# Optimization experiments

Measured on AMD Instinct MI355X. Metric: run time of the kernel, lower is better.

Reference implementation:

```python
import jax, jax.numpy as jnp
import numpy as np

A0 = 0.5291772105638411
KE = 14.399645351950548
KEHALF = KE / 2.0


def _softplus_inverse(x):
    return float(np.log(np.expm1(x)))


def setup_inputs() -> dict:
    key = jax.random.key(0)
    k_nb, k_mask, k_z, k_r = jax.random.split(key, 4)
    B, A, K = 16, 1024, 1023
    neighbors = jax.random.randint(k_nb, (B, A, K), 0, A)
    neighbor_mask = (jax.random.uniform(k_mask, (B, A, K)) > 0.1).astype(jnp.float32)
    atomic_numbers = jax.random.randint(k_z, (B, A), 1, 95)
    r_ij = jax.random.uniform(k_r, (B, A, K), minval=0.5, maxval=10.0, dtype=jnp.float32)
    p = jnp.float32
    params = {
        "_adiv": jnp.full((1,), _softplus_inverse(1.0 / (0.8854 * A0)), p),
        "_apow": jnp.full((1,), _softplus_inverse(0.23), p),
        "_c1": jnp.full((1,), _softplus_inverse(0.1818), p),
        "_c2": jnp.full((1,), _softplus_inverse(0.5099), p),
        "_c3": jnp.full((1,), _softplus_inverse(0.2802), p),
        "_c4": jnp.full((1,), _softplus_inverse(0.02817), p),
        "_a1": jnp.full((1,), _softplus_inverse(3.2), p),
        "_a2": jnp.full((1,), _softplus_inverse(0.9423), p),
        "_a3": jnp.full((1,), _softplus_inverse(0.4028), p),
        "_a4": jnp.full((1,), _softplus_inverse(0.2016), p),
    }
    return dict(neighbors=neighbors, neighbor_mask=neighbor_mask,
                atomic_numbers=atomic_numbers, r_ij=r_ij, **params)


def reference(neighbors, neighbor_mask, atomic_numbers, r_ij,
              _adiv, _apow, _c1, _c2, _c3, _c4, _a1, _a2, _a3, _a4):
    sp = jax.nn.softplus
    B = neighbors.shape[0]
    Zf = atomic_numbers.astype(jnp.float32)            # [B, A]
    Zp = Zf ** sp(_apow)                               # [B, A] (param [1] broadcasts)
    bidx = jnp.arange(B)[:, None, None]                # batch index for gather
    # gather of symmetric pair quantities without materializing [B, A, A]:
    # a[b,i,j] = Zp[b,i] + Zp[b,j];  zizj[b,i,j] = Zf[b,i] * Zf[b,j]
    Zp_j = Zp[bidx, neighbors]                         # [B, A, K]
    Zf_j = Zf[bidx, neighbors]                         # [B, A, K]
    a = (Zp[:, :, None] + Zp_j) * sp(_adiv) * neighbor_mask
    zizj = Zf[:, :, None] * Zf_j * neighbor_mask
    # normalized mixture coefficients
    c1, c2, c3, c4 = sp(_c1), sp(_c2), sp(_c3), sp(_c4)
    csum = c1 + c2 + c3 + c4
    c1, c2, c3, c4 = c1 / csum, c2 / csum, c3 / csum, c4 / csum
    ar = a * r_ij
    f = (c1 * jnp.exp(-sp(_a1) * ar) + c2 * jnp.exp(-sp(_a2) * ar)
         + c3 * jnp.exp(-sp(_a3) * ar) + c4 * jnp.exp(-sp(_a4) * ar))
    valid = neighbor_mask != 0
    r_safe = jnp.where(valid, r_ij, 1.0)
    corr_ij = jnp.where(valid, KEHALF * f * zizj / r_safe, 0.0)
    return jnp.sum(corr_ij, axis=-1, keepdims=True)    # [B, A, 1]
```

## Files before the change

### kernel.cpp

```cpp
#include <hip/hip_runtime.h>
#include <math.h>

#define KEHALF_F 7.199822675975274f

__device__ __forceinline__ float softplus_f(float x) {
    return log1pf(__expf(x));
}

__global__ __launch_bounds__(256) void zbl_precompute_kernel(
    const int* __restrict__ atomic_numbers,
    const float* __restrict__ p_adiv, const float* __restrict__ p_apow,
    const float* __restrict__ p_c1, const float* __restrict__ p_c2,
    const float* __restrict__ p_c3, const float* __restrict__ p_c4,
    const float* __restrict__ p_a1, const float* __restrict__ p_a2,
    const float* __restrict__ p_a3, const float* __restrict__ p_a4,
    float* __restrict__ ws, int n)
{
    int idx = blockIdx.x * blockDim.x + threadIdx.x;
    float sp_apow = softplus_f(p_apow[0]);
    if (idx == 0) {
        float c1 = softplus_f(p_c1[0]), c2 = softplus_f(p_c2[0]);
        float c3 = softplus_f(p_c3[0]), c4 = softplus_f(p_c4[0]);
        float cs = c1 + c2 + c3 + c4;
        ws[0] = softplus_f(p_adiv[0]);
        ws[1] = c1 / cs; ws[2] = c2 / cs; ws[3] = c3 / cs; ws[4] = c4 / cs;
        ws[5] = softplus_f(p_a1[0]); ws[6] = softplus_f(p_a2[0]);
        ws[7] = softplus_f(p_a3[0]); ws[8] = softplus_f(p_a4[0]);
    }
    if (idx < n) {
        float zf = (float)atomic_numbers[idx];
        ws[16 + idx] = powf(zf, sp_apow);
    }
}

__global__ __launch_bounds__(256) void zbl_main_kernel(
    const int* __restrict__ neighbors,
    const float* __restrict__ neighbor_mask,
    const int* __restrict__ atomic_numbers,
    const float* __restrict__ r_ij,
    const float* __restrict__ ws,
    float* __restrict__ out,
    int A, int K)
{
    __shared__ float2 zz[1024];
    __shared__ float wsum[4];

    const int row = blockIdx.x;
    const int b   = row / A;
    const int i   = row - b * A;

    const float* zp_row = ws + 16 + (size_t)b * A;
    const int*   z_row  = atomic_numbers + (size_t)b * A;
    for (int t = threadIdx.x; t < A; t += 256) {
        zz[t] = make_float2((float)z_row[t], zp_row[t]);
    }
    __syncthreads();

    const float sp_adiv = ws[0];
    const float c1 = ws[1], c2 = ws[2], c3 = ws[3], c4 = ws[4];
    const float a1 = ws[5], a2 = ws[6], a3 = ws[7], a4 = ws[8];

    const float2 zi = zz[i];

    const size_t base = (size_t)row * K;
    const int*   nb = neighbors     + base;
    const float* mk = neighbor_mask + base;
    const float* rr = r_ij          + base;

    float acc = 0.0f;
    for (int k = threadIdx.x; k < K; k += 256) {
        int   j = nb[k];
        float m = mk[k];
        float r = rr[k];
        float2 zj = zz[j];
        float am = (zi.y + zj.y) * sp_adiv * m;
        float ar = am * r;
        float f = c1 * __expf(-a1 * ar) + c2 * __expf(-a2 * ar)
                + c3 * __expf(-a3 * ar) + c4 * __expf(-a4 * ar);
        float zizj = zi.x * zj.x * m;
        acc += f * __fdividef(zizj, r);
    }
    acc *= KEHALF_F;

    #pragma unroll
    for (int off = 32; off > 0; off >>= 1)
        acc += __shfl_down(acc, off, 64);
    const int lane = threadIdx.x & 63;
    const int wid  = threadIdx.x >> 6;
    if (lane == 0) wsum[wid] = acc;
    __syncthreads();
    if (threadIdx.x == 0)
        out[row] = wsum[0] + wsum[1] + wsum[2] + wsum[3];
}

extern "C" void kernel_launch(void* const* d_in, const int* in_sizes, int n_in,
                              void* d_out, int out_size, void* d_ws, size_t ws_size,
                              hipStream_t stream) {
    const int*   neighbors      = (const int*)  d_in[0];
    const float* neighbor_mask  = (const float*)d_in[1];
    const int*   atomic_numbers = (const int*)  d_in[2];
    const float* r_ij           = (const float*)d_in[3];
    const float* p_adiv = (const float*)d_in[4];
    const float* p_apow = (const float*)d_in[5];
    const float* p_c1   = (const float*)d_in[6];
    const float* p_c2   = (const float*)d_in[7];
    const float* p_c3   = (const float*)d_in[8];
    const float* p_c4   = (const float*)d_in[9];
    const float* p_a1   = (const float*)d_in[10];
    const float* p_a2   = (const float*)d_in[11];
    const float* p_a3   = (const float*)d_in[12];
    const float* p_a4   = (const float*)d_in[13];

    float* out = (float*)d_out;
    float* ws  = (float*)d_ws;

    const int n = in_sizes[2];
    const int A = 1024;
    const int K = in_sizes[0] / n;

    zbl_precompute_kernel<<<(n + 255) / 256, 256, 0, stream>>>(
        atomic_numbers, p_adiv, p_apow, p_c1, p_c2, p_c3, p_c4,
        p_a1, p_a2, p_a3, p_a4, ws, n);

    zbl_main_kernel<<<n, 256, 0, stream>>>(
        neighbors, neighbor_mask, atomic_numbers, r_ij, ws, out, A, K);
}
```

Measured before the change: 219.7 us.

## Fuse precompute into main kernel and process eight rows per block

```diff
diff --git a/kernel.cpp b/kernel.cpp
--- a/kernel.cpp
+++ b/kernel.cpp
@@ -2,95 +2,98 @@
 #include <math.h>
 
 #define KEHALF_F 7.199822675975274f
+#define A_ATOMS 1024
+#define ROWS_PER_BLOCK 8
 
 __device__ __forceinline__ float softplus_f(float x) {
     return log1pf(__expf(x));
 }
 
-__global__ __launch_bounds__(256) void zbl_precompute_kernel(
+__global__ __launch_bounds__(256) void zbl_fused_kernel(
+    const int* __restrict__ neighbors,
+    const float* __restrict__ neighbor_mask,
     const int* __restrict__ atomic_numbers,
+    const float* __restrict__ r_ij,
     const float* __restrict__ p_adiv, const float* __restrict__ p_apow,
     const float* __restrict__ p_c1, const float* __restrict__ p_c2,
     const float* __restrict__ p_c3, const float* __restrict__ p_c4,
     const float* __restrict__ p_a1, const float* __restrict__ p_a2,
     const float* __restrict__ p_a3, const float* __restrict__ p_a4,
-    float* __restrict__ ws, int n)
+    float* __restrict__ out, int K)
 {
-    int idx = blockIdx.x * blockDim.x + threadIdx.x;
-    float sp_apow = softplus_f(p_apow[0]);
-    if (idx == 0) {
-        float c1 = softplus_f(p_c1[0]), c2 = softplus_f(p_c2[0]);
-        float c3 = softplus_f(p_c3[0]), c4 = softplus_f(p_c4[0]);
-        float cs = c1 + c2 + c3 + c4;
-        ws[0] = softplus_f(p_adiv[0]);
-        ws[1] = c1 / cs; ws[2] = c2 / cs; ws[3] = c3 / cs; ws[4] = c4 / cs;
-        ws[5] = softplus_f(p_a1[0]); ws[6] = softplus_f(p_a2[0]);
-        ws[7] = softplus_f(p_a3[0]); ws[8] = softplus_f(p_a4[0]);
-    }
-    if (idx < n) {
-        float zf = (float)atomic_numbers[idx];
-        ws[16 + idx] = powf(zf, sp_apow);
-    }
-}
+    __shared__ float2 zz[A_ATOMS];
 
-__global__ __launch_bounds__(256) void zbl_main_kernel(
-    const int* __restrict__ neighbors,
-    const float* __restrict__ neighbor_mask,
-    const int* __restrict__ atomic_numbers,
-    const float* __restrict__ r_ij,
-    const float* __restrict__ ws,
-    float* __restrict__ out,
-    int A, int K)
-{
-    __shared__ float2 zz[1024];
-    __shared__ float wsum[4];
+    const float sp_apow = softplus_f(p_apow[0]);
+    const float sp_adiv = softplus_f(p_adiv[0]);
+    float c1 = softplus_f(p_c1[0]), c2 = softplus_f(p_c2[0]);
+    float c3 = softplus_f(p_c3[0]), c4 = softplus_f(p_c4[0]);
+    const float inv_cs = 1.0f / (c1 + c2 + c3 + c4);
+    c1 *= inv_cs; c2 *= inv_cs; c3 *= inv_cs; c4 *= inv_cs;
+    const float a1 = softplus_f(p_a1[0]), a2 = softplus_f(p_a2[0]);
+    const float a3 = softplus_f(p_a3[0]), a4 = softplus_f(p_a4[0]);
 
-    const int row = blockIdx.x;
-    const int b   = row / A;
-    const int i   = row - b * A;
+    const int row_base = blockIdx.x * ROWS_PER_BLOCK;
+    const int b = row_base >> 10;
+    const int* z_row = atomic_numbers + (b << 10);
 
-    const float* zp_row = ws + 16 + (size_t)b * A;
-    const int*   z_row  = atomic_numbers + (size_t)b * A;
-    for (int t = threadIdx.x; t < A; t += 256) {
-        zz[t] = make_float2((float)z_row[t], zp_row[t]);
+    for (int t = threadIdx.x; t < A_ATOMS; t += 256) {
+        float zf = (float)z_row[t];
+        float zp = __expf(sp_apow * __logf(zf));
+        zz[t] = make_float2(zf, zp);
     }
     __syncthreads();
 
-    const float sp_adiv = ws[0];
-    const float c1 = ws[1], c2 = ws[2], c3 = ws[3], c4 = ws[4];
-    const float a1 = ws[5], a2 = ws[6], a3 = ws[7], a4 = ws[8];
+    const int wid  = threadIdx.x >> 6;
+    const int lane = threadIdx.x & 63;
 
-    const float2 zi = zz[i];
+    const int row0 = row_base + wid;
+    const int row1 = row_base + wid + 4;
+    const float2 zi0 = zz[row0 & (A_ATOMS - 1)];
+    const float2 zi1 = zz[row1 & (A_ATOMS - 1)];
 
-    const size_t base = (size_t)row * K;
-    const int*   nb = neighbors     + base;
-    const float* mk = neighbor_mask + base;
-    const float* rr = r_ij          + base;
+    const size_t base0 = (size_t)row0 * K;
+    const size_t base1 = (size_t)row1 * K;
+    const int*   nb0 = neighbors     + base0;
+    const float* mk0 = neighbor_mask + base0;
+    const float* rr0 = r_ij          + base0;
+    const int*   nb1 = neighbors     + base1;
+    const float* mk1 = neighbor_mask + base1;
+    const float* rr1 = r_ij          + base1;
 
-    float acc = 0.0f;
-    for (int k = threadIdx.x; k < K; k += 256) {
-        int   j = nb[k];
-        float m = mk[k];
-        float r = rr[k];
-        float2 zj = zz[j];
-        float am = (zi.y + zj.y) * sp_adiv * m;
-        float ar = am * r;
-        float f = c1 * __expf(-a1 * ar) + c2 * __expf(-a2 * ar)
-                + c3 * __expf(-a3 * ar) + c4 * __expf(-a4 * ar);
-        float zizj = zi.x * zj.x * m;
-        acc += f * __fdividef(zizj, r);
+    float acc0 = 0.0f, acc1 = 0.0f;
+    const int niter = (K + 63) >> 6;
+    #pragma unroll 4
+    for (int it = 0; it < niter; ++it) {
+        const int k = (it << 6) + lane;
+        if (k < K) {
+            int   j0 = nb0[k];
+            float m0 = mk0[k];
+            float r0 = rr0[k];
+            float2 zj0 = zz[j0];
+            float ar0 = (zi0.y + zj0.y) * sp_adiv * m0 * r0;
+            float f0  = c1 * __expf(-a1 * ar0) + c2 * __expf(-a2 * ar0)
+                      + c3 * __expf(-a3 * ar0) + c4 * __expf(-a4 * ar0);
+            acc0 += f0 * __fdividef(zi0.x * zj0.x * m0, r0);
+            int   j1 = nb1[k];
+            float m1 = mk1[k];
+            float r1 = rr1[k];
+            float2 zj1 = zz[j1];
+            float ar1 = (zi1.y + zj1.y) * sp_adiv * m1 * r1;
+            float f1  = c1 * __expf(-a1 * ar1) + c2 * __expf(-a2 * ar1)
+                      + c3 * __expf(-a3 * ar1) + c4 * __expf(-a4 * ar1);
+            acc1 += f1 * __fdividef(zi1.x * zj1.x * m1, r1);
+        }
     }
-    acc *= KEHALF_F;
 
     #pragma unroll
-    for (int off = 32; off > 0; off >>= 1)
-        acc += __shfl_down(acc, off, 64);
-    const int lane = threadIdx.x & 63;
-    const int wid  = threadIdx.x >> 6;
-    if (lane == 0) wsum[wid] = acc;
-    __syncthreads();
-    if (threadIdx.x == 0)
-        out[row] = wsum[0] + wsum[1] + wsum[2] + wsum[3];
+    for (int off = 32; off > 0; off >>= 1) {
+        acc0 += __shfl_down(acc0, off, 64);
+        acc1 += __shfl_down(acc1, off, 64);
+    }
+    if (lane == 0) {
+        out[row0] = KEHALF_F * acc0;
+        out[row1] = KEHALF_F * acc1;
+    }
 }
 
 extern "C" void kernel_launch(void* const* d_in, const int* in_sizes, int n_in,
@@ -100,28 +103,18 @@
     const float* neighbor_mask  = (const float*)d_in[1];
     const int*   atomic_numbers = (const int*)  d_in[2];
     const float* r_ij           = (const float*)d_in[3];
-    const float* p_adiv = (const float*)d_in[4];
-    const float* p_apow = (const float*)d_in[5];
-    const float* p_c1   = (const float*)d_in[6];
-    const float* p_c2   = (const float*)d_in[7];
-    const float* p_c3   = (const float*)d_in[8];
-    const float* p_c4   = (const float*)d_in[9];
-    const float* p_a1   = (const float*)d_in[10];
-    const float* p_a2   = (const float*)d_in[11];
-    const float* p_a3   = (const float*)d_in[12];
-    const float* p_a4   = (const float*)d_in[13];
 
     float* out = (float*)d_out;
-    float* ws  = (float*)d_ws;
 
     const int n = in_sizes[2];
-    const int A = 1024;
     const int K = in_sizes[0] / n;
 
-    zbl_precompute_kernel<<<(n + 255) / 256, 256, 0, stream>>>(
-        atomic_numbers, p_adiv, p_apow, p_c1, p_c2, p_c3, p_c4,
-        p_a1, p_a2, p_a3, p_a4, ws, n);
-
-    zbl_main_kernel<<<n, 256, 0, stream>>>(
-        neighbors, neighbor_mask, atomic_numbers, r_ij, ws, out, A, K);
+    zbl_fused_kernel<<<n / ROWS_PER_BLOCK, 256, 0, stream>>>(
+        neighbors, neighbor_mask, atomic_numbers, r_ij,
+        (const float*)d_in[4], (const float*)d_in[5],
+        (const float*)d_in[6], (const float*)d_in[7],
+        (const float*)d_in[8], (const float*)d_in[9],
+        (const float*)d_in[10], (const float*)d_in[11],
+        (const float*)d_in[12], (const float*)d_in[13],
+        out, K);
 }
```

After: 235.3 us. 1.07x slower.
